# Kernel tuning notes

Measured on AMD Instinct MI355X. Metric: run time of the kernel, lower is better.

## Reference

```python
import jax, jax.numpy as jnp
import numpy as np

IGNORE_INDEX = 255
RATIO = 0.2


def setup_inputs() -> dict:
    key = jax.random.key(0)
    pred = jax.random.normal(key, (4, 19, 512, 1024), dtype=jnp.float32)
    return {"pred": pred}


def reference(pred):
    # pred: [N, C, H, W] logits
    N, C, H, W = pred.shape
    prob = jax.nn.softmax(pred, axis=1)                      # [N, C, H, W]
    # maxpred is softmax output in (0,1) so the != ignore_index masks are all True;
    # argpred is the per-pixel predicted class.
    argpred = jnp.argmax(prob, axis=1)                        # [N, H, W] int
    labels = argpred.reshape(N, H * W)                        # [N, HW]

    # torch.histc(label, bins=C+1, min=-1, max=C-1)[1:] on integer labels 0..C-1
    # is exactly a per-class bincount (value v lands in bin v+1).
    hist = jnp.zeros((N, C), dtype=prob.dtype).at[
        jnp.arange(N)[:, None], labels
    ].add(1.0)                                               # [N, C] class counts

    total = jnp.asarray(H * W, dtype=prob.dtype)             # hist.sum() per sample
    class_w = 1.0 / jnp.maximum(
        jnp.power(hist, RATIO) * jnp.power(total, 1.0 - RATIO), 1.0
    )                                                        # [N, C]

    # gather per-pixel weight of the argmax class; detached in the original
    pix_w = jnp.take_along_axis(class_w, labels, axis=1)     # [N, HW]
    pix_w = jax.lax.stop_gradient(pix_w.reshape(N, 1, H, W))  # [N, 1, H, W]

    loss = -jnp.sum(jnp.square(prob) * pix_w) / (N * C)
    return loss
```

## Files before the change

kernel.cpp:

```cpp
#include <hip/hip_runtime.h>

#define NB   4
#define C    19
#define HW   (512 * 1024)
#define BPN  256
#define NBLK (NB * BPN)
#define SLOT BPN
#define ITER 4
#define NBIN (NB * C)

__global__ __launch_bounds__(256) void msql_pass1(
    const float* __restrict__ pred,
    float2* __restrict__ part)
{
    __shared__ float    s_ssum[C];
    __shared__ unsigned s_cnt[C];
    const int tid = threadIdx.x;
    if (tid < C) { s_ssum[tid] = 0.0f; s_cnt[tid] = 0u; }
    __syncthreads();

    const unsigned b  = blockIdx.x;
    const unsigned n  = b >> 8;
    const unsigned lb = b & (BPN - 1u);
    const float* nbase = pred + (size_t)n * ((size_t)C * HW);

#pragma unroll 1
    for (int it = 0; it < ITER; ++it) {
        const unsigned p2 = lb * (256u * ITER) + (unsigned)it * 256u + (unsigned)tid;
        const float* base = nbase + (size_t)p2 * 2;

        float2 x[C];
#pragma unroll
        for (int c = 0; c < C; ++c)
            x[c] = *reinterpret_cast<const float2*>(base + (size_t)c * HW);

#pragma unroll
        for (int j = 0; j < 2; ++j) {
            float m  = j ? x[0].y : x[0].x;
            int  arg = 0;
#pragma unroll
            for (int c = 1; c < C; ++c) {
                float v = j ? x[c].y : x[c].x;
                if (v > m) { m = v; arg = c; }
            }
            float s1 = 0.0f, s2 = 0.0f;
#pragma unroll
            for (int c = 0; c < C; ++c) {
                float e = __expf((j ? x[c].y : x[c].x) - m);
                s1 += e;
                s2 = fmaf(e, e, s2);
            }
            const float S = s2 / (s1 * s1);
            atomicAdd(&s_ssum[arg], S);
            atomicAdd(&s_cnt[arg], 1u);
        }
    }

    __syncthreads();
    if (tid < C) {
        part[(((unsigned)tid * NB + n) << 8) + lb] =
            make_float2(s_ssum[tid], (float)s_cnt[tid]);
    }
}

__global__ __launch_bounds__(1024) void msql_tail(
    const float2* __restrict__ part,
    float* __restrict__ out)
{
    __shared__ float l_val[NBIN];
    const int t    = threadIdx.x;
    const int w    = t >> 6;
    const int lane = t & 63;

    for (int bin = w; bin < NBIN; bin += 16) {
        const float2* p = part + ((size_t)bin << 8);
        float ss = 0.0f, cc = 0.0f;
#pragma unroll
        for (int i = 0; i < SLOT / 64; ++i) {
            float2 v = p[lane + (i << 6)];
            ss += v.x; cc += v.y;
        }
#pragma unroll
        for (int off = 32; off > 0; off >>= 1) {
            ss += __shfl_down(ss, off, 64);
            cc += __shfl_down(cc, off, 64);
        }
        if (lane == 0) {
            float denom = fmaxf(powf(cc, 0.2f) * powf((float)HW, 0.8f), 1.0f);
            l_val[bin] = ss / denom;
        }
    }
    __syncthreads();
    if (w == 0) {
        float v = l_val[lane];
        if (lane < NBIN - 64) v += l_val[lane + 64];
#pragma unroll
        for (int off = 32; off > 0; off >>= 1)
            v += __shfl_down(v, off, 64);
        if (lane == 0)
            out[0] = -v / (float)NBIN;
    }
}

extern "C" void kernel_launch(void* const* d_in, const int* in_sizes, int n_in,
                              void* d_out, int out_size, void* d_ws, size_t ws_size,
                              hipStream_t stream) {
    const float* pred = (const float*)d_in[0];
    float*  out  = (float*)d_out;
    float2* part = (float2*)d_ws;

    msql_pass1<<<dim3(NBLK), dim3(256), 0, stream>>>(pred, part);
    msql_tail <<<dim3(1),    dim3(1024), 0, stream>>>(part, out);
}
```

Measured before the change: 38.09 us.

## Stream classes with online softmax over float4 pixels per thread

Pass one now walks the 19 classes once and keeps a running max, argmax, sum of exponentials and sum of squared exponentials for each pixel, replacing the load-all-then-two-pass scheme. Each thread handles four pixels with float4 loads instead of two pixels over four iterations, and the grid doubles to 512 blocks per sample, each covering 1024 pixels. The aim is to cut register pressure, raise occupancy (launch bounds now ask for 6 blocks) and widen loads on a bandwidth-bound kernel. The cost is two exponentials per element instead of one, and the tail kernel must now reduce twice as many partials.

```diff
diff --git a/kernel.cpp b/kernel.cpp
--- a/kernel.cpp
+++ b/kernel.cpp
@@ -3,13 +3,12 @@
 #define NB   4
 #define C    19
 #define HW   (512 * 1024)
-#define BPN  256
+#define BPN  512
 #define NBLK (NB * BPN)
-#define SLOT BPN
-#define ITER 4
+#define PXB  1024
 #define NBIN (NB * C)
 
-__global__ __launch_bounds__(256) void msql_pass1(
+__global__ __launch_bounds__(256, 6) void msql_pass1(
     const float* __restrict__ pred,
     float2* __restrict__ part)
 {
@@ -20,45 +19,48 @@
     __syncthreads();
 
     const unsigned b  = blockIdx.x;
-    const unsigned n  = b >> 8;
+    const unsigned n  = b >> 9;
     const unsigned lb = b & (BPN - 1u);
-    const float* nbase = pred + (size_t)n * ((size_t)C * HW);
+    const float* base = pred + (size_t)n * ((size_t)C * HW)
+                             + (size_t)lb * PXB + (size_t)tid * 4;
 
-#pragma unroll 1
-    for (int it = 0; it < ITER; ++it) {
-        const unsigned p2 = lb * (256u * ITER) + (unsigned)it * 256u + (unsigned)tid;
-        const float* base = nbase + (size_t)p2 * 2;
+    float m[4], s1[4], s2[4];
+    int   arg[4];
+    {
+        float4 v = *reinterpret_cast<const float4*>(base);
+        m[0] = v.x; m[1] = v.y; m[2] = v.z; m[3] = v.w;
+#pragma unroll
+        for (int j = 0; j < 4; ++j) { s1[j] = 1.0f; s2[j] = 1.0f; arg[j] = 0; }
+    }
 
-        float2 x[C];
+#pragma unroll 2
+    for (int c = 1; c < C; ++c) {
+        float4 v = *reinterpret_cast<const float4*>(base + (size_t)c * HW);
+        float vv[4] = { v.x, v.y, v.z, v.w };
 #pragma unroll
-        for (int c = 0; c < C; ++c)
-            x[c] = *reinterpret_cast<const float2*>(base + (size_t)c * HW);
+        for (int j = 0; j < 4; ++j) {
+            float x  = vv[j];
+            bool  gt = x > m[j];
+            float mn = gt ? x : m[j];
+            float sc = __expf(m[j] - mn);
+            float e  = __expf(x - mn);
+            s1[j] = fmaf(s1[j], sc, e);
+            s2[j] = fmaf(s2[j] * sc, sc, e * e);
+            m[j]  = mn;
+            arg[j] = gt ? c : arg[j];
+        }
+    }
 
 #pragma unroll
-        for (int j = 0; j < 2; ++j) {
-            float m  = j ? x[0].y : x[0].x;
-            int  arg = 0;
-#pragma unroll
-            for (int c = 1; c < C; ++c) {
-                float v = j ? x[c].y : x[c].x;
-                if (v > m) { m = v; arg = c; }
-            }
-            float s1 = 0.0f, s2 = 0.0f;
-#pragma unroll
-            for (int c = 0; c < C; ++c) {
-                float e = __expf((j ? x[c].y : x[c].x) - m);
-                s1 += e;
-                s2 = fmaf(e, e, s2);
-            }
-            const float S = s2 / (s1 * s1);
-            atomicAdd(&s_ssum[arg], S);
-            atomicAdd(&s_cnt[arg], 1u);
-        }
+    for (int j = 0; j < 4; ++j) {
+        float S = s2[j] / (s1[j] * s1[j]);
+        atomicAdd(&s_ssum[arg[j]], S);
+        atomicAdd(&s_cnt[arg[j]], 1u);
     }
 
     __syncthreads();
     if (tid < C) {
-        part[(((unsigned)tid * NB + n) << 8) + lb] =
+        part[(((unsigned)tid * NB + n) << 9) + lb] =
             make_float2(s_ssum[tid], (float)s_cnt[tid]);
     }
 }
@@ -73,10 +75,10 @@
     const int lane = t & 63;
 
     for (int bin = w; bin < NBIN; bin += 16) {
-        const float2* p = part + ((size_t)bin << 8);
+        const float2* p = part + ((size_t)bin << 9);
         float ss = 0.0f, cc = 0.0f;
 #pragma unroll
-        for (int i = 0; i < SLOT / 64; ++i) {
+        for (int i = 0; i < BPN / 64; ++i) {
             float2 v = p[lane + (i << 6)];
             ss += v.x; cc += v.y;
         }
```

Result: slower. 45.18 us (+18.6%).
